# Kernel optimization log

Hardware: AMD Instinct MI355X
Metric: run time of the kernel (lower is better)

## Reference

```python
import jax, jax.numpy as jnp
import numpy as np

SELF_DIM = 6
GS_DIM = 100

def _lin(x, w, b):
    return x @ w + b

def setup_inputs() -> dict:
    key = jax.random.key(0)
    ks = jax.random.split(key, 24)
    def p(k, shape, fan_in):
        return jax.random.normal(k, shape, dtype=jnp.float32) * (1.0 / np.sqrt(fan_in))
    state = jax.random.normal(ks[0], (16384, 20, 13), dtype=jnp.float32)
    inp = {"state": state}
    # mlp1: 13 -> 150 -> 100 -> 100
    inp["w1"], inp["b1"] = p(ks[1], (13, 150), 13), jnp.zeros((150,), jnp.float32)
    inp["w2"], inp["b2"] = p(ks[2], (150, 100), 150), jnp.zeros((100,), jnp.float32)
    inp["w3"], inp["b3"] = p(ks[3], (100, 100), 100), jnp.zeros((100,), jnp.float32)
    # attention: 200 -> 100 -> 100 -> 1
    inp["a1"], inp["ab1"] = p(ks[4], (200, 100), 200), jnp.zeros((100,), jnp.float32)
    inp["a2"], inp["ab2"] = p(ks[5], (100, 100), 100), jnp.zeros((100,), jnp.float32)
    inp["a3"], inp["ab3"] = p(ks[6], (100, 1), 100), jnp.zeros((1,), jnp.float32)
    # mlp2: 106 -> 150 -> 100 -> 100 -> 1
    inp["m1"], inp["mb1"] = p(ks[7], (106, 150), 106), jnp.zeros((150,), jnp.float32)
    inp["m2"], inp["mb2"] = p(ks[8], (150, 100), 150), jnp.zeros((100,), jnp.float32)
    inp["m3"], inp["mb3"] = p(ks[9], (100, 100), 100), jnp.zeros((100,), jnp.float32)
    inp["m4"], inp["mb4"] = p(ks[10], (100, 1), 100), jnp.zeros((1,), jnp.float32)
    return inp

def reference(state, w1, b1, w2, b2, w3, b3, a1, ab1, a2, ab2, a3, ab3,
              m1, mb1, m2, mb2, m3, mb3, m4, mb4):
    B, N, D = state.shape
    self_state = state[:, 0, :SELF_DIM]                      # [B, 6]
    x = state.reshape(B * N, D)
    h = jax.nn.relu(_lin(x, w1, b1))
    h = jax.nn.relu(_lin(h, w2, b2))
    mlp1_out = _lin(h, w3, b3)                               # [B*N, 100]
    feat = mlp1_out.reshape(B, N, GS_DIM)
    global_state = jnp.broadcast_to(feat.mean(axis=1, keepdims=True), (B, N, GS_DIM))
    att_in = jnp.concatenate([feat, global_state], axis=-1)  # [B, N, 200]
    s = jax.nn.relu(_lin(att_in, a1, ab1))
    s = jax.nn.relu(_lin(s, a2, ab2))
    scores = jax.nn.relu(_lin(s, a3, ab3))[..., 0]           # [B, N]
    weights = jax.nn.softmax(scores, axis=1)                 # [B, N]
    weighted_feature = jnp.einsum('bn,bnd->bd', weights, feat)
    joint = jnp.concatenate([self_state, weighted_feature], axis=-1)  # [B, 106]
    v = jax.nn.relu(_lin(joint, m1, mb1))
    v = jax.nn.relu(_lin(v, m2, mb2))
    v = jax.nn.relu(_lin(v, m3, mb3))
    value = _lin(v, m4, mb4)                                 # [B, 1]
    return value
```

## Files before the change

### kernel.cpp

```cpp
#include <hip/hip_runtime.h>
#include <math.h>

#define NTHR 512
#define NB 4
#define NROWSR (NB * 20)

typedef _Float16 h8v __attribute__((ext_vector_type(8)));
using f4 = __attribute__((ext_vector_type(4))) float;

#define H1_OFF 0
#define H1_PK 168
#define H2_OFF 26880
#define H2_PK 136
#define FEAT_OFF 0
#define FEAT_PK 136
#define S1_OFF 26880
#define S1_PK 136
#define XS_OFF 26880
#define XS_PK 40
#define GS_OFF S1_OFF
#define POOL1 48640

#define L1B 0
#define L2B 20
#define L3B 90
#define A1B 146
#define A2B 202
#define M1B 258
#define M2B 338
#define M3B 408
#define A1GB 464
#define JOINT_F 133120

#define K2ROWS 64
#define K2THR 256
#define K2_JT_OFF 0
#define K2_V1_OFF 17408
#define K2_POOL 38912

__device__ __forceinline__ float relu_f(float v) { return fmaxf(v, 0.f); }
__device__ __forceinline__ float h2f(ushort u) {
  return (float)__builtin_bit_cast(_Float16, u);
}
__device__ __forceinline__ ushort f2h(float v) {
  return __builtin_bit_cast(ushort, (_Float16)v);
}
__device__ __forceinline__ uint pk2h(float a, float b) {
  return (uint)f2h(a) | ((uint)f2h(b) << 16);
}

__device__ __forceinline__ float4 load4_guard(const float* __restrict__ a, int of4, int C) {
  float4 v;
  if (of4 + 3 < C) v = *(const float4*)(a + of4);
  else {
    v.x = (of4 + 0 < C) ? a[of4 + 0] : 0.f;
    v.y = (of4 + 1 < C) ? a[of4 + 1] : 0.f;
    v.z = (of4 + 2 < C) ? a[of4 + 2] : 0.f;
    v.w = (of4 + 3 < C) ? a[of4 + 3] : 0.f;
  }
  return v;
}

__global__ __launch_bounds__(64) void prep_kernel(
    const float* __restrict__ w1, const float* __restrict__ w2,
    const float* __restrict__ w3, const float* __restrict__ a1,
    const float* __restrict__ a2, const float* __restrict__ m1,
    const float* __restrict__ m2, const float* __restrict__ m3,
    uint4* __restrict__ ws) {
  const int job = blockIdx.x;
  const int lane = threadIdx.x;
  const float* W;
  int K, C, NT, base, kb, nt, i;
  if (job < 10)       { W = w1; K = 13;  C = 150; NT = 10; base = L1B; kb = 0; nt = job; }
  else if (job < 45)  { W = w2; K = 150; C = 100; NT = 7;  base = L2B; i = job - 10;  kb = i / 7;  nt = i % 7; }
  else if (job < 73)  { W = w3; K = 100; C = 100; NT = 7;  base = L3B; i = job - 45;  kb = i / 7;  nt = i % 7; }
  else if (job < 101) { W = a1; K = 100; C = 100; NT = 7;  base = A1B; i = job - 73;  kb = i / 7;  nt = i % 7; }
  else if (job < 129) { W = a2; K = 100; C = 100; NT = 7;  base = A2B; i = job - 101; kb = i / 7;  nt = i % 7; }
  else if (job < 169) { W = m1; K = 106; C = 150; NT = 10; base = M1B; i = job - 129; kb = i / 10; nt = i % 10; }
  else if (job < 204) { W = m2; K = 150; C = 100; NT = 7;  base = M2B; i = job - 169; kb = i / 7;  nt = i % 7; }
  else if (job < 232) { W = m3; K = 100; C = 100; NT = 7;  base = M3B; i = job - 204; kb = i / 7;  nt = i % 7; }
  else                { W = a1 + 10000; K = 100; C = 100; NT = 7; base = A1GB; i = job - 232; kb = i / 7; nt = i % 7; }
  const int r = lane & 15, g = lane >> 4;
  const int j = nt * 16 + r;
  uint hi[8], lo[8];
  for (int e = 0; e < 8; ++e) {
    int k = kb * 32 + g * 8 + e;
    float v = (k < K && j < C) ? W[k * C + j] : 0.f;
    _Float16 hh = (_Float16)v;
    float hf = (float)hh;
    _Float16 ll = (_Float16)(v - hf);
    hi[e] = (uint)__builtin_bit_cast(ushort, hh);
    lo[e] = (uint)__builtin_bit_cast(ushort, ll);
  }
  uint4 vh = { hi[0] | (hi[1] << 16), hi[2] | (hi[3] << 16),
               hi[4] | (hi[5] << 16), hi[6] | (hi[7] << 16) };
  uint4 vl = { lo[0] | (lo[1] << 16), lo[2] | (lo[3] << 16),
               lo[4] | (lo[5] << 16), lo[6] | (lo[7] << 16) };
  ws[(size_t)(base + (kb * NT + nt) * 2 + 0) * 64 + lane] = vh;
  ws[(size_t)(base + (kb * NT + nt) * 2 + 1) * 64 + lane] = vl;
}

template <int KB, int NT, int C, int MODE, int ROWS, bool W8, int TERMS>
__device__ __forceinline__ void mfma_layer(
    char* pool, int inOff, int PKin, int outOff, int PKout,
    const h8v* __restrict__ wsB, const float* __restrict__ bias,
    const float* gpartL, float* sceL, const float* __restrict__ a3,
    int lane, int wid) {
  constexpr int MTL = ROWS / 16;
  const int r = lane & 15, g = lane >> 4;
  const char* Ain = pool + inOff;
  int wlo, mtb, mte;
  if constexpr (W8) {
    wlo = wid & 3;
    const int whi = wid >> 2;
    mtb = whi ? 3 : 0; mte = whi ? MTL : 3;
  } else { wlo = wid; mtb = 0; mte = MTL; }
  for (int nt = wlo; nt < NT; nt += 4) {
    h8v wh[KB], wl[KB];
#pragma unroll
    for (int kb = 0; kb < KB; ++kb) {
      wh[kb] = wsB[((kb * NT + nt) * 2 + 0) * 64 + lane];
      if constexpr (TERMS == 2)
        wl[kb] = wsB[((kb * NT + nt) * 2 + 1) * 64 + lane];
    }
    const int of = nt * 16 + g * 4;
    const float4 b4 = load4_guard(bias, of, C);
    float4 a34 = {0.f, 0.f, 0.f, 0.f};
    if constexpr (MODE == 3) a34 = load4_guard(a3, of, C);
    for (int mt = mtb; mt < mte; ++mt) {
      const int ar = mt * 16 + r;
      f4 acc = {0.f, 0.f, 0.f, 0.f};
      const char* aP = Ain + ar * (PKin * 2) + g * 16;
#pragma unroll
      for (int kb = 0; kb < KB; ++kb) {
        h8v a = *(const h8v*)(aP + kb * 64);
        acc = __builtin_amdgcn_mfma_f32_16x16x32_f16(wh[kb], a, acc, 0, 0, 0);
        if constexpr (TERMS == 2)
          acc = __builtin_amdgcn_mfma_f32_16x16x32_f16(wl[kb], a, acc, 0, 0, 0);
      }
      float v0, v1, v2, v3;
      if constexpr (MODE == 2) {
        const float* gpb = gpartL + (ar / 20) * 100;
        float4 gp4 = (of + 3 < C) ? *(const float4*)(gpb + of)
                                  : load4_guard(gpb, of, C);
        v0 = acc[0] + b4.x + gp4.x; v1 = acc[1] + b4.y + gp4.y;
        v2 = acc[2] + b4.z + gp4.z; v3 = acc[3] + b4.w + gp4.w;
      } else {
        v0 = acc[0] + b4.x; v1 = acc[1] + b4.y;
        v2 = acc[2] + b4.z; v3 = acc[3] + b4.w;
      }
      if constexpr (MODE != 1) {
        v0 = fmaxf(v0, 0.f); v1 = fmaxf(v1, 0.f);
        v2 = fmaxf(v2, 0.f); v3 = fmaxf(v3, 0.f);
      }
      if constexpr (MODE == 3) {
        float val = v0 * a34.x + v1 * a34.y + v2 * a34.z + v3 * a34.w;
        val += __shfl_xor(val, 16);
        val += __shfl_xor(val, 32);
        if (lane < 16) atomicAdd(&sceL[ar], val);
      } else {
        uint2 pk = { pk2h(v0, v1), pk2h(v2, v3) };
        *(uint2*)((ushort*)(pool + outOff) + ar * PKout + of) = pk;
      }
    }
  }
}

template <int ROWSZ, int PK>
__device__ __forceinline__ void zero_tail(char* pool, int off, int tid) {
  if (tid < ROWSZ) {
    uint4* z = (uint4*)((ushort*)(pool + off) + (size_t)tid * PK + 112);
    z[0] = uint4{0, 0, 0, 0};
    z[1] = uint4{0, 0, 0, 0};
  }
}

__global__ __launch_bounds__(NTHR, 6) void value_net_kernel(
    const float* __restrict__ state,
    const float* __restrict__ b1, const float* __restrict__ b2,
    const float* __restrict__ b3,
    const float* __restrict__ ab1, const float* __restrict__ ab2,
    const float* __restrict__ a3, const float* __restrict__ ab3,
    const uint4* __restrict__ ws, float* __restrict__ jointg) {
  __shared__ char pool[POOL1];
  __shared__ float gpartL[NB * 100], sceL[NROWSR], swL[NROWSR];

  const int tid = threadIdx.x;
  const int lane = tid & 63, wid = tid >> 6;
  const int b0 = blockIdx.x * NB;
  const h8v* wsb = (const h8v*)ws;

  for (int i = tid; i < NROWSR * XS_PK; i += NTHR) {
    int row = i / XS_PK, k = i - row * XS_PK;
    float v = (k < 13) ? state[((size_t)b0 * 20 + row) * 13 + k] : 0.f;
    ((ushort*)(pool + XS_OFF))[row * XS_PK + k] = f2h(v);
  }
  if (tid < NROWSR) sceL[tid] = 0.f;
  __syncthreads();

  mfma_layer<1, 10, 150, 0, NROWSR, true, 1>(
      pool, XS_OFF, XS_PK, H1_OFF, H1_PK, wsb + L1B * 64, b1,
      nullptr, nullptr, nullptr, lane, wid);
  __syncthreads();

  zero_tail<NROWSR, H2_PK>(pool, H2_OFF, tid);
  mfma_layer<5, 7, 100, 0, NROWSR, true, 1>(
      pool, H1_OFF, H1_PK, H2_OFF, H2_PK, wsb + L2B * 64, b2,
      nullptr, nullptr, nullptr, lane, wid);
  __syncthreads();

  zero_tail<NROWSR, FEAT_PK>(pool, FEAT_OFF, tid);
  mfma_layer<4, 7, 100, 1, NROWSR, true, 1>(
      pool, H2_OFF, H2_PK, FEAT_OFF, FEAT_PK, wsb + L3B * 64, b3,
      nullptr, nullptr, nullptr, lane, wid);
  __syncthreads();

  if (tid < NB * 100) {
    const int b = tid / 100, d = tid - b * 100;
    const ushort* f = (const ushort*)(pool + FEAT_OFF);
    float s = 0.f;
    for (int n = 0; n < 20; ++n) s += h2f(f[(b * 20 + n) * FEAT_PK + d]);
    ((ushort*)(pool + GS_OFF))[b * 136 + d] = f2h(s * 0.05f);
  } else if (tid < NB * 100 + NB * 28) {
    const int idx = tid - NB * 100;
    ((ushort*)(pool + GS_OFF))[(idx / 28) * 136 + 100 + (idx % 28)] = 0;
  }
  __syncthreads();

  if (wid < 7) {
    const int r = lane & 15, g = lane >> 4;
    const int nt = wid;
    const h8v* wsg = wsb + A1GB * 64;
    h8v wh[4];
#pragma unroll
    for (int kb = 0; kb < 4; ++kb)
      wh[kb] = wsg[((kb * 7 + nt) * 2 + 0) * 64 + lane];
    const char* aP = pool + GS_OFF + (r & 3) * (136 * 2) + g * 16;
    f4 acc = {0.f, 0.f, 0.f, 0.f};
#pragma unroll
    for (int kb = 0; kb < 4; ++kb) {
      h8v a = *(const h8v*)(aP + kb * 64);
      acc = __builtin_amdgcn_mfma_f32_16x16x32_f16(wh[kb], a, acc, 0, 0, 0);
    }
    const int of = nt * 16 + g * 4;
    if (r < 4 && of < 100) {
      *(float4*)(&gpartL[r * 100 + of]) = float4{acc[0], acc[1], acc[2], acc[3]};
    }
  }
  __syncthreads();

  mfma_layer<4, 7, 100, 2, NROWSR, true, 1>(
      pool, FEAT_OFF, FEAT_PK, S1_OFF, S1_PK, wsb + A1B * 64, ab1,
      gpartL, nullptr, nullptr, lane, wid);
  __syncthreads();

  mfma_layer<4, 7, 100, 3, NROWSR, true, 1>(
      pool, S1_OFF, S1_PK, 0, 0, wsb + A2B * 64, ab2,
      nullptr, sceL, a3, lane, wid);
  __syncthreads();

  if (tid < NROWSR) {
    const int b = tid / 20, n = tid - b * 20;
    const float ab3v = ab3[0];
    float m = -1e30f;
    for (int i = 0; i < 20; ++i) m = fmaxf(m, relu_f(sceL[b * 20 + i] + ab3v));
    float sum = 0.f, mine = 0.f;
    for (int i = 0; i < 20; ++i) {
      float e = __expf(relu_f(sceL[b * 20 + i] + ab3v) - m);
      sum += e;
      if (i == n) mine = e;
    }
    swL[tid] = mine / sum;
  }
  __syncthreads();

  for (int it = tid; it < NB * 200; it += NTHR) {
    const int b = it / 200, rem = it - b * 200;
    const int d = rem >> 1, half = rem & 1;
    const ushort* f = (const ushort*)(pool + FEAT_OFF);
    float acc = 0.f;
    for (int n = half * 10; n < half * 10 + 10; ++n)
      acc += swL[b * 20 + n] * h2f(f[(b * 20 + n) * FEAT_PK + d]);
    acc += __shfl_xor(acc, 1);
    if (half == 0) jointg[(size_t)(b0 + b) * 106 + 6 + d] = acc;
  }
  if (tid < NB * 6) {
    const int b = tid / 6, i = tid - b * 6;
    jointg[(size_t)(b0 + b) * 106 + i] = state[((size_t)(b0 + b)) * 260 + i];
  }
}

__global__ __launch_bounds__(K2THR) void mlp2_kernel(
    const float* __restrict__ jointg,
    const float* __restrict__ mb1, const float* __restrict__ mb2,
    const float* __restrict__ mb3,
    const float* __restrict__ m4, const float* __restrict__ mb4,
    const uint4* __restrict__ ws, float* __restrict__ out) {
  __shared__ char pool[K2_POOL];
  __shared__ float m4L[100];
  const int tid = threadIdx.x, lane = tid & 63, wid = tid >> 6;
  const size_t r0 = (size_t)blockIdx.x * K2ROWS;
  const h8v* wsb = (const h8v*)ws;

  for (int i = tid; i < K2ROWS * 136; i += K2THR) {
    int row = i / 136, k = i - row * 136;
    float v = (k < 106) ? jointg[(r0 + row) * 106 + k] : 0.f;
    ((ushort*)(pool + K2_JT_OFF))[row * 136 + k] = f2h(v);
  }
  if (tid < 100) m4L[tid] = m4[tid];
  __syncthreads();

  mfma_layer<4, 10, 150, 0, K2ROWS, false, 2>(
      pool, K2_JT_OFF, 136, K2_V1_OFF, 168, wsb + M1B * 64, mb1,
      nullptr, nullptr, nullptr, lane, wid);
  __syncthreads();

  zero_tail<K2ROWS, 136>(pool, 0, tid);
  mfma_layer<5, 7, 100, 0, K2ROWS, false, 2>(
      pool, K2_V1_OFF, 168, 0, 136, wsb + M2B * 64, mb2,
      nullptr, nullptr, nullptr, lane, wid);
  __syncthreads();

  mfma_layer<4, 7, 100, 0, K2ROWS, false, 2>(
      pool, 0, 136, K2_V1_OFF, 136, wsb + M3B * 64, mb3,
      nullptr, nullptr, nullptr, lane, wid);
  __syncthreads();

  {
    const int row = tid >> 2, seg = tid & 3;
    const ushort* v3 = (const ushort*)(pool + K2_V1_OFF);
    float s = 0.f;
    for (int k = seg; k < 100; k += 4) s += h2f(v3[row * 136 + k]) * m4L[k];
    s += __shfl_xor(s, 1);
    s += __shfl_xor(s, 2);
    if (seg == 0) out[r0 + row] = s + mb4[0];
  }
}

extern "C" void kernel_launch(void* const* d_in, const int* in_sizes, int n_in,
                              void* d_out, int out_size, void* d_ws, size_t ws_size,
                              hipStream_t stream) {
  const float* state = (const float*)d_in[0];
  const float* w1 = (const float*)d_in[1];
  const float* b1 = (const float*)d_in[2];
  const float* w2 = (const float*)d_in[3];
  const float* b2 = (const float*)d_in[4];
  const float* w3 = (const float*)d_in[5];
  const float* b3 = (const float*)d_in[6];
  const float* a1 = (const float*)d_in[7];
  const float* ab1 = (const float*)d_in[8];
  const float* a2 = (const float*)d_in[9];
  const float* ab2 = (const float*)d_in[10];
  const float* a3 = (const float*)d_in[11];
  const float* ab3 = (const float*)d_in[12];
  const float* m1 = (const float*)d_in[13];
  const float* mb1 = (const float*)d_in[14];
  const float* m2 = (const float*)d_in[15];
  const float* mb2 = (const float*)d_in[16];
  const float* m3 = (const float*)d_in[17];
  const float* mb3 = (const float*)d_in[18];
  const float* m4 = (const float*)d_in[19];
  const float* mb4 = (const float*)d_in[20];
  float* out = (float*)d_out;
  uint4* ws = (uint4*)d_ws;
  float* jointg = (float*)d_ws + JOINT_F;

  prep_kernel<<<260, 64, 0, stream>>>(w1, w2, w3, a1, a2, m1, m2, m3, ws);

  const int B = in_sizes[0] / 260;
  value_net_kernel<<<dim3(B / NB), dim3(NTHR), 0, stream>>>(
      state, b1, b2, b3, ab1, ab2, a3, ab3, (const uint4*)ws, jointg);

  mlp2_kernel<<<dim3(B / K2ROWS), dim3(K2THR), 0, stream>>>(
      jointg, mb1, mb2, mb3, m4, mb4, (const uint4*)ws, out);
}
```

Measured before the change: 129.5 us.

## Move layer epilogues to packed fp16 math and store joint features as fp16

A new prep block converts the bias vectors to padded fp16 arrays in the workspace. Layer epilogues then convert MFMA accumulators to fp16 first and do bias add, global-part add and ReLU as packed half2 operations, which drops the per-element float bias loads and guards. The global-state partials and the intermediate joint buffer between the two kernels become fp16, halving that global traffic. The per-batch softmax is rewritten as a warp-shuffle reduction. The cost is extra rounding before the bias add and in the stored joint features, which may reduce accuracy.

```diff
diff --git a/kernel.cpp b/kernel.cpp
--- a/kernel.cpp
+++ b/kernel.cpp
@@ -6,7 +6,12 @@
 #define NROWSR (NB * 20)
 
 typedef _Float16 h8v __attribute__((ext_vector_type(8)));
+typedef _Float16 h2v __attribute__((ext_vector_type(2)));
 using f4 = __attribute__((ext_vector_type(4))) float;
+
+__device__ __forceinline__ h2v cvt_pk_h2(float a, float b) {
+  return __builtin_bit_cast(h2v, __builtin_amdgcn_cvt_pkrtz(a, b));
+}
 
 #define H1_OFF 0
 #define H1_PK 168
@@ -30,7 +35,16 @@
 #define M2B 338
 #define M3B 408
 #define A1GB 464
-#define JOINT_F 133120
+#define BIAS_BYTE 532480
+#define JOINT_BYTE 536576
+
+#define BO_B1 0
+#define BO_B2 160
+#define BO_B3 320
+#define BO_AB1 480
+#define BO_MB1 800
+#define BO_MB2 960
+#define BO_MB3 1120
 
 #define K2ROWS 64
 #define K2THR 256
@@ -66,9 +80,32 @@
     const float* __restrict__ w3, const float* __restrict__ a1,
     const float* __restrict__ a2, const float* __restrict__ m1,
     const float* __restrict__ m2, const float* __restrict__ m3,
+    const float* __restrict__ b1, const float* __restrict__ b2,
+    const float* __restrict__ b3, const float* __restrict__ ab1,
+    const float* __restrict__ mb1, const float* __restrict__ mb2,
+    const float* __restrict__ mb3,
     uint4* __restrict__ ws) {
   const int job = blockIdx.x;
   const int lane = threadIdx.x;
+  if (job == 260) {
+    ushort* bh = (ushort*)((char*)ws + BIAS_BYTE);
+    for (int idx = lane; idx < 1280; idx += 64) {
+      const int reg = idx / 160, off = idx - reg * 160;
+      const float* src = nullptr; int C = 0;
+      switch (reg) {
+        case 0: src = b1;  C = 150; break;
+        case 1: src = b2;  C = 100; break;
+        case 2: src = b3;  C = 100; break;
+        case 3: src = ab1; C = 100; break;
+        case 4: src = nullptr; C = 0; break;
+        case 5: src = mb1; C = 150; break;
+        case 6: src = mb2; C = 100; break;
+        default: src = mb3; C = 100; break;
+      }
+      bh[idx] = (off < C) ? f2h(src[off]) : (ushort)0;
+    }
+    return;
+  }
   const float* W;
   int K, C, NT, base, kb, nt, i;
   if (job < 10)       { W = w1; K = 13;  C = 150; NT = 10; base = L1B; kb = 0; nt = job; }
@@ -103,9 +140,9 @@
 template <int KB, int NT, int C, int MODE, int ROWS, bool W8, int TERMS>
 __device__ __forceinline__ void mfma_layer(
     char* pool, int inOff, int PKin, int outOff, int PKout,
-    const h8v* __restrict__ wsB, const float* __restrict__ bias,
-    const float* gpartL, float* sceL, const float* __restrict__ a3,
-    int lane, int wid) {
+    const h8v* __restrict__ wsB, const ushort* __restrict__ biasH,
+    const float* __restrict__ biasF, const ushort* gpartH, float* sceL,
+    const float* __restrict__ a3, int lane, int wid) {
   constexpr int MTL = ROWS / 16;
   const int r = lane & 15, g = lane >> 4;
   const char* Ain = pool + inOff;
@@ -124,9 +161,14 @@
         wl[kb] = wsB[((kb * NT + nt) * 2 + 1) * 64 + lane];
     }
     const int of = nt * 16 + g * 4;
-    const float4 b4 = load4_guard(bias, of, C);
-    float4 a34 = {0.f, 0.f, 0.f, 0.f};
-    if constexpr (MODE == 3) a34 = load4_guard(a3, of, C);
+    uint2 bp;
+    float4 b4, a34;
+    if constexpr (MODE == 3) {
+      b4 = load4_guard(biasF, of, C);
+      a34 = load4_guard(a3, of, C);
+    } else {
+      bp = *(const uint2*)(biasH + of);
+    }
     for (int mt = mtb; mt < mte; ++mt) {
       const int ar = mt * 16 + r;
       f4 acc = {0.f, 0.f, 0.f, 0.f};
@@ -138,29 +180,30 @@
         if constexpr (TERMS == 2)
           acc = __builtin_amdgcn_mfma_f32_16x16x32_f16(wl[kb], a, acc, 0, 0, 0);
       }
-      float v0, v1, v2, v3;
-      if constexpr (MODE == 2) {
-        const float* gpb = gpartL + (ar / 20) * 100;
-        float4 gp4 = (of + 3 < C) ? *(const float4*)(gpb + of)
-                                  : load4_guard(gpb, of, C);
-        v0 = acc[0] + b4.x + gp4.x; v1 = acc[1] + b4.y + gp4.y;
-        v2 = acc[2] + b4.z + gp4.z; v3 = acc[3] + b4.w + gp4.w;
-      } else {
-        v0 = acc[0] + b4.x; v1 = acc[1] + b4.y;
-        v2 = acc[2] + b4.z; v3 = acc[3] + b4.w;
-      }
-      if constexpr (MODE != 1) {
-        v0 = fmaxf(v0, 0.f); v1 = fmaxf(v1, 0.f);
-        v2 = fmaxf(v2, 0.f); v3 = fmaxf(v3, 0.f);
-      }
       if constexpr (MODE == 3) {
+        float v0 = fmaxf(acc[0] + b4.x, 0.f), v1 = fmaxf(acc[1] + b4.y, 0.f);
+        float v2 = fmaxf(acc[2] + b4.z, 0.f), v3 = fmaxf(acc[3] + b4.w, 0.f);
         float val = v0 * a34.x + v1 * a34.y + v2 * a34.z + v3 * a34.w;
         val += __shfl_xor(val, 16);
         val += __shfl_xor(val, 32);
         if (lane < 16) atomicAdd(&sceL[ar], val);
       } else {
-        uint2 pk = { pk2h(v0, v1), pk2h(v2, v3) };
-        *(uint2*)((ushort*)(pool + outOff) + ar * PKout + of) = pk;
+        h2v lo = cvt_pk_h2(acc[0], acc[1]);
+        h2v hi = cvt_pk_h2(acc[2], acc[3]);
+        lo += __builtin_bit_cast(h2v, bp.x);
+        hi += __builtin_bit_cast(h2v, bp.y);
+        if constexpr (MODE == 2) {
+          uint2 gp = *(const uint2*)(gpartH + (ar / 20) * 112 + of);
+          lo += __builtin_bit_cast(h2v, gp.x);
+          hi += __builtin_bit_cast(h2v, gp.y);
+        }
+        if constexpr (MODE != 1) {
+          h2v z = {(_Float16)0.f, (_Float16)0.f};
+          lo = __builtin_elementwise_max(lo, z);
+          hi = __builtin_elementwise_max(hi, z);
+        }
+        *(uint2*)((ushort*)(pool + outOff) + ar * PKout + of) =
+            uint2{__builtin_bit_cast(uint, lo), __builtin_bit_cast(uint, hi)};
       }
     }
   }
@@ -177,18 +220,18 @@
 
 __global__ __launch_bounds__(NTHR, 6) void value_net_kernel(
     const float* __restrict__ state,
-    const float* __restrict__ b1, const float* __restrict__ b2,
-    const float* __restrict__ b3,
-    const float* __restrict__ ab1, const float* __restrict__ ab2,
+    const float* __restrict__ ab2,
     const float* __restrict__ a3, const float* __restrict__ ab3,
-    const uint4* __restrict__ ws, float* __restrict__ jointg) {
+    const uint4* __restrict__ ws, ushort* __restrict__ jointgH) {
   __shared__ char pool[POOL1];
-  __shared__ float gpartL[NB * 100], sceL[NROWSR], swL[NROWSR];
+  __shared__ ushort gpartH[NB * 112];
+  __shared__ float sceL[NROWSR], swL[NROWSR];
 
   const int tid = threadIdx.x;
   const int lane = tid & 63, wid = tid >> 6;
   const int b0 = blockIdx.x * NB;
   const h8v* wsb = (const h8v*)ws;
+  const ushort* biasH = (const ushort*)((const char*)ws + BIAS_BYTE);
 
   for (int i = tid; i < NROWSR * XS_PK; i += NTHR) {
     int row = i / XS_PK, k = i - row * XS_PK;
@@ -199,20 +242,20 @@
   __syncthreads();
 
   mfma_layer<1, 10, 150, 0, NROWSR, true, 1>(
-      pool, XS_OFF, XS_PK, H1_OFF, H1_PK, wsb + L1B * 64, b1,
-      nullptr, nullptr, nullptr, lane, wid);
+      pool, XS_OFF, XS_PK, H1_OFF, H1_PK, wsb + L1B * 64, biasH + BO_B1,
+      nullptr, nullptr, nullptr, nullptr, lane, wid);
   __syncthreads();
 
   zero_tail<NROWSR, H2_PK>(pool, H2_OFF, tid);
   mfma_layer<5, 7, 100, 0, NROWSR, true, 1>(
-      pool, H1_OFF, H1_PK, H2_OFF, H2_PK, wsb + L2B * 64, b2,
-      nullptr, nullptr, nullptr, lane, wid);
+      pool, H1_OFF, H1_PK, H2_OFF, H2_PK, wsb + L2B * 64, biasH + BO_B2,
+      nullptr, nullptr, nullptr, nullptr, lane, wid);
   __syncthreads();
 
   zero_tail<NROWSR, FEAT_PK>(pool, FEAT_OFF, tid);
   mfma_layer<4, 7, 100, 1, NROWSR, true, 1>(
-      pool, H2_OFF, H2_PK, FEAT_OFF, FEAT_PK, wsb + L3B * 64, b3,
-      nullptr, nullptr, nullptr, lane, wid);
+      pool, H2_OFF, H2_PK, FEAT_OFF, FEAT_PK, wsb + L3B * 64, biasH + BO_B3,
+      nullptr, nullptr, nullptr, nullptr, lane, wid);
   __syncthreads();
 
   if (tid < NB * 100) {
@@ -243,34 +286,35 @@
       acc = __builtin_amdgcn_mfma_f32_16x16x32_f16(wh[kb], a, acc, 0, 0, 0);
     }
     const int of = nt * 16 + g * 4;
-    if (r < 4 && of < 100) {
-      *(float4*)(&gpartL[r * 100 + of]) = float4{acc[0], acc[1], acc[2], acc[3]};
+    if (r < 4) {
+      uint2 pk = { pk2h(acc[0], acc[1]), pk2h(acc[2], acc[3]) };
+      *(uint2*)(gpartH + r * 112 + of) = pk;
     }
   }
   __syncthreads();
 
   mfma_layer<4, 7, 100, 2, NROWSR, true, 1>(
-      pool, FEAT_OFF, FEAT_PK, S1_OFF, S1_PK, wsb + A1B * 64, ab1,
-      gpartL, nullptr, nullptr, lane, wid);
+      pool, FEAT_OFF, FEAT_PK, S1_OFF, S1_PK, wsb + A1B * 64, biasH + BO_AB1,
+      nullptr, gpartH, nullptr, nullptr, lane, wid);
   __syncthreads();
 
   mfma_layer<4, 7, 100, 3, NROWSR, true, 1>(
-      pool, S1_OFF, S1_PK, 0, 0, wsb + A2B * 64, ab2,
-      nullptr, sceL, a3, lane, wid);
-  __syncthreads();
-
-  if (tid < NROWSR) {
-    const int b = tid / 20, n = tid - b * 20;
+      pool, S1_OFF, S1_PK, 0, 0, wsb + A2B * 64, nullptr,
+      ab2, nullptr, sceL, a3, lane, wid);
+  __syncthreads();
+
+  if (tid < 128) {
+    const int b = tid >> 5, l = tid & 31;
     const float ab3v = ab3[0];
-    float m = -1e30f;
-    for (int i = 0; i < 20; ++i) m = fmaxf(m, relu_f(sceL[b * 20 + i] + ab3v));
-    float sum = 0.f, mine = 0.f;
-    for (int i = 0; i < 20; ++i) {
-      float e = __expf(relu_f(sceL[b * 20 + i] + ab3v) - m);
-      sum += e;
-      if (i == n) mine = e;
-    }
-    swL[tid] = mine / sum;
+    float s = (l < 20) ? relu_f(sceL[b * 20 + l] + ab3v) : -1e30f;
+    float m = s;
+#pragma unroll
+    for (int d = 1; d < 32; d <<= 1) m = fmaxf(m, __shfl_xor(m, d));
+    float e = (l < 20) ? __expf(s - m) : 0.f;
+    float sum = e;
+#pragma unroll
+    for (int d = 1; d < 32; d <<= 1) sum += __shfl_xor(sum, d);
+    if (l < 20) swL[b * 20 + l] = e / sum;
   }
   __syncthreads();
 
@@ -282,18 +326,16 @@
     for (int n = half * 10; n < half * 10 + 10; ++n)
       acc += swL[b * 20 + n] * h2f(f[(b * 20 + n) * FEAT_PK + d]);
     acc += __shfl_xor(acc, 1);
-    if (half == 0) jointg[(size_t)(b0 + b) * 106 + 6 + d] = acc;
+    if (half == 0) jointgH[(size_t)(b0 + b) * 106 + 6 + d] = f2h(acc);
   }
   if (tid < NB * 6) {
     const int b = tid / 6, i = tid - b * 6;
-    jointg[(size_t)(b0 + b) * 106 + i] = state[((size_t)(b0 + b)) * 260 + i];
+    jointgH[(size_t)(b0 + b) * 106 + i] = f2h(state[((size_t)(b0 + b)) * 260 + i]);
   }
 }
 
 __global__ __launch_bounds__(K2THR) void mlp2_kernel(
-    const float* __restrict__ jointg,
-    const float* __restrict__ mb1, const float* __restrict__ mb2,
-    const float* __restrict__ mb3,
+    const ushort* __restrict__ jointgH,
     const float* __restrict__ m4, const float* __restrict__ mb4,
     const uint4* __restrict__ ws, float* __restrict__ out) {
   __shared__ char pool[K2_POOL];
@@ -301,29 +343,30 @@
   const int tid = threadIdx.x, lane = tid & 63, wid = tid >> 6;
   const size_t r0 = (size_t)blockIdx.x * K2ROWS;
   const h8v* wsb = (const h8v*)ws;
+  const ushort* biasH = (const ushort*)((const char*)ws + BIAS_BYTE);
 
   for (int i = tid; i < K2ROWS * 136; i += K2THR) {
     int row = i / 136, k = i - row * 136;
-    float v = (k < 106) ? jointg[(r0 + row) * 106 + k] : 0.f;
-    ((ushort*)(pool + K2_JT_OFF))[row * 136 + k] = f2h(v);
+    ((ushort*)(pool + K2_JT_OFF))[row * 136 + k] =
+        (k < 106) ? jointgH[(r0 + row) * 106 + k] : (ushort)0;
   }
   if (tid < 100) m4L[tid] = m4[tid];
   __syncthreads();
 
   mfma_layer<4, 10, 150, 0, K2ROWS, false, 2>(
-      pool, K2_JT_OFF, 136, K2_V1_OFF, 168, wsb + M1B * 64, mb1,
-      nullptr, nullptr, nullptr, lane, wid);
+      pool, K2_JT_OFF, 136, K2_V1_OFF, 168, wsb + M1B * 64, biasH + BO_MB1,
+      nullptr, nullptr, nullptr, nullptr, lane, wid);
   __syncthreads();
 
   zero_tail<K2ROWS, 136>(pool, 0, tid);
   mfma_layer<5, 7, 100, 0, K2ROWS, false, 2>(
-      pool, K2_V1_OFF, 168, 0, 136, wsb + M2B * 64, mb2,
-      nullptr, nullptr, nullptr, lane, wid);
+      pool, K2_V1_OFF, 168, 0, 136, wsb + M2B * 64, biasH + BO_MB2,
+      nullptr, nullptr, nullptr, nullptr, lane, wid);
   __syncthreads();
 
   mfma_layer<4, 7, 100, 0, K2ROWS, false, 2>(
-      pool, 0, 136, K2_V1_OFF, 136, wsb + M3B * 64, mb3,
-      nullptr, nullptr, nullptr, lane, wid);
+      pool, 0, 136, K2_V1_OFF, 136, wsb + M3B * 64, biasH + BO_MB3,
+      nullptr, nullptr, nullptr, nullptr, lane, wid);
   __syncthreads();
 
   {
@@ -363,14 +406,15 @@
   const float* mb4 = (const float*)d_in[20];
   float* out = (float*)d_out;
   uint4* ws = (uint4*)d_ws;
-  float* jointg = (float*)d_ws + JOINT_F;
-
-  prep_kernel<<<260, 64, 0, stream>>>(w1, w2, w3, a1, a2, m1, m2, m3, ws);
+  ushort* jointgH = (ushort*)((char*)d_ws + JOINT_BYTE);
+
+  prep_kernel<<<261, 64, 0, stream>>>(w1, w2, w3, a1, a2, m1, m2, m3,
+                                      b1, b2, b3, ab1, mb1, mb2, mb3, ws);
 
   const int B = in_sizes[0] / 260;
   value_net_kernel<<<dim3(B / NB), dim3(NTHR), 0, stream>>>(
-      state, b1, b2, b3, ab1, ab2, a3, ab3, (const uint4*)ws, jointg);
+      state, ab2, a3, ab3, (const uint4*)ws, jointgH);
 
   mlp2_kernel<<<dim3(B / K2ROWS), dim3(K2THR), 0, stream>>>(
-      jointg, mb1, mb2, mb3, m4, mb4, (const uint4*)ws, out);
-}
+      jointgH, m4, mb4, (const uint4*)ws, out);
+}
```

Result: faster. 123.8 us (-4.4%).
